# Optimization experiments

Hardware: AMD Instinct MI355X
Metric: run time of the kernel (lower is better)

## Reference

```python
import jax, jax.numpy as jnp
import numpy as np

NUM_CLASSES = 1000
FEAT_DIM = 512
BATCH = 16384


def setup_inputs() -> dict:
    key = jax.random.key(0)
    k1, k2, k3 = jax.random.split(key, 3)
    x = jax.random.normal(k1, (BATCH, FEAT_DIM), dtype=jnp.float32)
    labels = jax.random.randint(k2, (BATCH,), 0, NUM_CLASSES, dtype=jnp.int64)
    centers = jax.random.normal(k3, (NUM_CLASSES, FEAT_DIM), dtype=jnp.float32)
    margin = jnp.ones((1,), dtype=jnp.float32)
    return {"x": x, "labels": labels, "centers": centers, "margin": margin}


def reference(x, labels, centers, margin):
    # squared euclidean distances: [B, C]
    distmat = (
        jnp.sum(x * x, axis=1, keepdims=True)
        + jnp.sum(centers * centers, axis=1)[None, :]
        - 2.0 * (x @ centers.T)
    )
    B, C = distmat.shape
    onehot = labels[:, None] == jnp.arange(C, dtype=labels.dtype)[None, :]  # [B, C]
    # distance to the true-class center
    dist = jnp.sum(jnp.where(onehot, distmat, 0.0), axis=1)  # [B]
    # min distance over all other classes (mask true class with +inf)
    dist_min = jnp.min(jnp.where(onehot, jnp.inf, distmat), axis=1)  # [B]
    m = margin[0]
    loss = jnp.sum(jnp.maximum(m + dist - dist_min, 0.0)) / B
    return loss
```

## Files before the change

kernel.cpp:

```cpp
#include <hip/hip_runtime.h>
#include <hip/hip_bf16.h>

#define BATCH 16384
#define NCLS  1000
#define NPAD  1024
#define FDIM  512

#define CBLK_STRIDE 266240
#define TAIL_OFF    262144
#define XBLK_STRIDE 262144

typedef __bf16 bf16x8 __attribute__((ext_vector_type(8)));
typedef float  f32x16 __attribute__((ext_vector_type(16)));

#define GLOBAL_AS __attribute__((address_space(1)))
#define LDS_AS    __attribute__((address_space(3)))

#define VMCNT(n) asm volatile("s_waitcnt vmcnt(" #n ")" ::: "memory")
#define LGKM0()  asm volatile("s_waitcnt lgkmcnt(0)" ::: "memory")
#define SBAR()   __builtin_amdgcn_s_barrier()
#define SCHED0() __builtin_amdgcn_sched_barrier(0)

__global__ __launch_bounds__(256) void prep(
    const float* __restrict__ centers, const float* __restrict__ x,
    char* __restrict__ cbt, char* __restrict__ xbt, float* __restrict__ out)
{
    const int bid = blockIdx.x, t = threadIdx.x;
    if (bid == 0 && t == 0) out[0] = 0.f;

    if (bid < 256) {
        const int lane = t & 63;
        const int c = bid * 4 + (t >> 6);
        const int cblk = c >> 8, cl = c & 255;
        char* base = cbt + (size_t)cblk * CBLK_STRIDE;

        float4 f0 = make_float4(0.f, 0.f, 0.f, 0.f);
        float4 f1 = make_float4(0.f, 0.f, 0.f, 0.f);
        if (c < NCLS) {
            f0 = *(const float4*)(centers + (size_t)c * FDIM + lane * 8);
            f1 = *(const float4*)(centers + (size_t)c * FDIM + lane * 8 + 4);
        }
        bf16x8 b;
        b[0] = (__bf16)f0.x; b[1] = (__bf16)f0.y; b[2] = (__bf16)f0.z; b[3] = (__bf16)f0.w;
        b[4] = (__bf16)f1.x; b[5] = (__bf16)f1.y; b[6] = (__bf16)f1.z; b[7] = (__bf16)f1.w;
        *(bf16x8*)(base + (lane >> 3) * 32768 + (lane & 7) * 4096 + cl * 16) = b;

        float ssum = f0.x*f0.x + f0.y*f0.y + f0.z*f0.z + f0.w*f0.w
                   + f1.x*f1.x + f1.y*f1.y + f1.z*f1.z + f1.w*f1.w;
        #pragma unroll
        for (int o = 32; o > 0; o >>= 1) ssum += __shfl_down(ssum, o);
        if (lane == 0) {
            const float hf = (c < NCLS) ? (-0.5f * ssum) : -1e30f;
            const __bf16 h = (__bf16)hf;
            const __bf16 l = (c < NCLS) ? (__bf16)(hf - (float)h) : (__bf16)0.f;
            bf16x8 tl;
            #pragma unroll
            for (int e = 0; e < 8; ++e) tl[e] = (__bf16)0.f;
            tl[0] = h; tl[1] = l;
            *(bf16x8*)(base + TAIL_OFF + cl * 16) = tl;
        }
    } else {
        const int pid  = bid - 256;
        const int bblk = pid >> 3, s = pid & 7;
        const float* src = x + (size_t)(bblk * 256 + t) * FDIM + s * 64;
        float4 f[16];
        #pragma unroll
        for (int j = 0; j < 16; ++j) f[j] = *(const float4*)(src + j * 4);
        char* dst = xbt + (size_t)bblk * XBLK_STRIDE + s * 32768 + t * 16;
        #pragma unroll
        for (int c = 0; c < 8; ++c) {
            bf16x8 b;
            b[0] = (__bf16)f[c*2].x;   b[1] = (__bf16)f[c*2].y;
            b[2] = (__bf16)f[c*2].z;   b[3] = (__bf16)f[c*2].w;
            b[4] = (__bf16)f[c*2+1].x; b[5] = (__bf16)f[c*2+1].y;
            b[6] = (__bf16)f[c*2+1].z; b[7] = (__bf16)f[c*2+1].w;
            *(bf16x8*)(dst + c * 4096) = b;
        }
    }
}

__global__ __launch_bounds__(512, 1) void trip_main(
    const int* __restrict__ labels, const char* __restrict__ cbt,
    const char* __restrict__ xbt, float* __restrict__ mxp,
    float* __restrict__ dap)
{
    extern __shared__ char lds[];
    const int t    = threadIdx.x;
    const int lane = t & 63;
    const int w    = t >> 6;
    const int wN   = w & 3, wM = w >> 2;
    const int l31  = lane & 31, hi = lane >> 5;
    const int bid  = blockIdx.x;
    const int cblk = bid >> 6;
    const int bblk = bid & 63;
    const int class0 = cblk * 256;
    const int row0   = bblk * 256;
    const char* cbB  = cbt + (size_t)cblk * CBLK_STRIDE;
    const char* xbB  = xbt + (size_t)bblk * XBLK_STRIDE;

    auto stageAu = [&](int T, int u) {
        const int off = u * 8192 + t * 16;
        __builtin_amdgcn_global_load_lds(
            (const GLOBAL_AS void*)(cbB + T * 32768 + off),
            (LDS_AS void*)(lds + (T & 1) * 32768 + off), 16, 0, 0);
    };

    f32x16 acc[4][2];
    #pragma unroll
    for (int mi = 0; mi < 4; ++mi)
        #pragma unroll
        for (int ni = 0; ni < 2; ++ni)
            #pragma unroll
            for (int r = 0; r < 16; ++r) acc[mi][ni][r] = 0.f;

    bf16x8 bE[4][2], bO[4][2];

    const int lab0 = labels[row0 + wN * 64 + l31];
    const int lab1 = labels[row0 + wN * 64 + 32 + l31];
    if (t < 256) {
        const char* src = cbB + TAIL_OFF + t * 16;
        char* dst = lds + 65536 + t * 16;
        __builtin_amdgcn_global_load_lds((const GLOBAL_AS void*)src,
                                         (LDS_AS void*)dst, 16, 0, 0);
    }
    #pragma unroll
    for (int u = 0; u < 4; ++u) stageAu(0, u);
    #pragma unroll
    for (int u = 0; u < 4; ++u) {
        const char* bsrc = xbB + (u * 2 + hi) * 4096 + (wN * 64 + l31) * 16;
        bE[u][0] = *(const bf16x8*)(bsrc);
        bE[u][1] = *(const bf16x8*)(bsrc + 512);
    }
    VMCNT(0);
    SBAR(); SCHED0();

    #pragma unroll
    for (int T = 0; T < 8; ++T) {
        const char* A = lds + (T & 1) * 32768;
        auto& bCur = (T & 1) ? bO : bE;
        auto& bNxt = (T & 1) ? bE : bO;
        #pragma unroll
        for (int u = 0; u < 4; ++u) {
            if (T < 7)       { VMCNT(6); }
            else if (u == 0) { VMCNT(6); }
            else if (u == 1) { VMCNT(3); }
            else if (u == 2) { VMCNT(0); }
            const int chunk = u * 2 + hi;
            bf16x8 a0 = *(const bf16x8*)(A + chunk * 4096 + (wM * 128 +  0 + l31) * 16);
            bf16x8 a1 = *(const bf16x8*)(A + chunk * 4096 + (wM * 128 + 32 + l31) * 16);
            bf16x8 a2 = *(const bf16x8*)(A + chunk * 4096 + (wM * 128 + 64 + l31) * 16);
            bf16x8 a3 = *(const bf16x8*)(A + chunk * 4096 + (wM * 128 + 96 + l31) * 16);
            if (T < 7) {
                stageAu(T + 1, u);
                const char* bsrc = xbB + (T + 1) * 32768 + chunk * 4096
                                 + (wN * 64 + l31) * 16;
                bNxt[u][0] = *(const bf16x8*)(bsrc);
                bNxt[u][1] = *(const bf16x8*)(bsrc + 512);
            }
            SBAR();
            LGKM0();
            SCHED0();
            __builtin_amdgcn_s_setprio(1);
            acc[0][0] = __builtin_amdgcn_mfma_f32_32x32x16_bf16(a0, bCur[u][0], acc[0][0], 0, 0, 0);
            acc[0][1] = __builtin_amdgcn_mfma_f32_32x32x16_bf16(a0, bCur[u][1], acc[0][1], 0, 0, 0);
            acc[1][0] = __builtin_amdgcn_mfma_f32_32x32x16_bf16(a1, bCur[u][0], acc[1][0], 0, 0, 0);
            acc[1][1] = __builtin_amdgcn_mfma_f32_32x32x16_bf16(a1, bCur[u][1], acc[1][1], 0, 0, 0);
            acc[2][0] = __builtin_amdgcn_mfma_f32_32x32x16_bf16(a2, bCur[u][0], acc[2][0], 0, 0, 0);
            acc[2][1] = __builtin_amdgcn_mfma_f32_32x32x16_bf16(a2, bCur[u][1], acc[2][1], 0, 0, 0);
            acc[3][0] = __builtin_amdgcn_mfma_f32_32x32x16_bf16(a3, bCur[u][0], acc[3][0], 0, 0, 0);
            acc[3][1] = __builtin_amdgcn_mfma_f32_32x32x16_bf16(a3, bCur[u][1], acc[3][1], 0, 0, 0);
            __builtin_amdgcn_s_setprio(0);
            SBAR();
            SCHED0();
        }
    }

    {
        const char* T = lds + 65536;
        bf16x8 bt;
        #pragma unroll
        for (int e = 0; e < 8; ++e) bt[e] = (__bf16)0.f;
        if (hi == 0) { bt[0] = (__bf16)1.0f; bt[1] = (__bf16)1.0f; }
        #pragma unroll
        for (int mi = 0; mi < 4; ++mi) {
            bf16x8 a = *(const bf16x8*)(T + (wM * 128 + mi * 32 + l31) * 16);
            #pragma unroll
            for (int ni = 0; ni < 2; ++ni)
                acc[mi][ni] = __builtin_amdgcn_mfma_f32_32x32x16_bf16(
                    a, bt, acc[mi][ni], 0, 0, 0);
        }
    }

    const int labBase = class0 + wM * 128 + hi * 4;
    const int labA0 = lab0 - labBase;
    const int labA1 = lab1 - labBase;
    float MX0 = -3e38f, MX1 = -3e38f, DA0 = -3e38f, DA1 = -3e38f;
    #pragma unroll
    for (int mi = 0; mi < 4; ++mi) {
        #pragma unroll
        for (int r = 0; r < 16; ++r) {
            const int pat = mi * 32 + (r & 3) + 8 * (r >> 2);
            {
                const float a = acc[mi][0][r];
                const bool is = (labA0 == pat);
                MX0 = fmaxf(MX0, is ? -3e38f : a);
                DA0 = is ? a : DA0;
            }
            {
                const float a = acc[mi][1][r];
                const bool is = (labA1 == pat);
                MX1 = fmaxf(MX1, is ? -3e38f : a);
                DA1 = is ? a : DA1;
            }
        }
    }
    MX0 = fmaxf(MX0, __shfl_xor(MX0, 32));
    DA0 = fmaxf(DA0, __shfl_xor(DA0, 32));
    MX1 = fmaxf(MX1, __shfl_xor(MX1, 32));
    DA1 = fmaxf(DA1, __shfl_xor(DA1, 32));

    float* sc = (float*)lds;
    const int i0 = (wN * 2 + 0) * 32 + l31;
    const int i1 = (wN * 2 + 1) * 32 + l31;
    __syncthreads();
    if (wM == 1 && hi == 0) {
        sc[i0] = MX0; sc[256 + i0] = DA0;
        sc[i1] = MX1; sc[256 + i1] = DA1;
    }
    __syncthreads();
    if (wM == 0 && hi == 0) {
        const float M0 = fmaxf(MX0, sc[i0]),  D0 = fmaxf(DA0, sc[256 + i0]);
        const float M1 = fmaxf(MX1, sc[i1]),  D1 = fmaxf(DA1, sc[256 + i1]);
        const int rg = row0 + wN * 64 + l31;
        mxp[cblk * BATCH + rg]      = M0;
        dap[cblk * BATCH + rg]      = D0;
        mxp[cblk * BATCH + rg + 32] = M1;
        dap[cblk * BATCH + rg + 32] = D1;
    }
}

__global__ __launch_bounds__(256) void combine(
    const float* __restrict__ mxp, const float* __restrict__ dap,
    const float* __restrict__ margin, float* __restrict__ out)
{
    const int t = threadIdx.x;
    const int row = blockIdx.x * 256 + t;
    float mx = fmaxf(fmaxf(mxp[row], mxp[BATCH + row]),
                     fmaxf(mxp[2 * BATCH + row], mxp[3 * BATCH + row]));
    float da = fmaxf(fmaxf(dap[row], dap[BATCH + row]),
                     fmaxf(dap[2 * BATCH + row], dap[3 * BATCH + row]));
    float loss = fmaxf(margin[0] - 2.f * da + 2.f * mx, 0.f);
    __shared__ float red[4];
    #pragma unroll
    for (int o = 32; o > 0; o >>= 1) loss += __shfl_down(loss, o);
    if ((t & 63) == 0) red[t >> 6] = loss;
    __syncthreads();
    if (t == 0)
        atomicAdd(out, (red[0] + red[1] + red[2] + red[3]) * (1.0f / BATCH));
}

extern "C" void kernel_launch(void* const* d_in, const int* in_sizes, int n_in,
                              void* d_out, int out_size, void* d_ws, size_t ws_size,
                              hipStream_t stream)
{
    const float* x       = (const float*)d_in[0];
    const int*   labels  = (const int*)d_in[1];
    const float* centers = (const float*)d_in[2];
    const float* margin  = (const float*)d_in[3];
    float* out = (float*)d_out;

    char* ws = (char*)d_ws;
    char*  cbt  = ws;
    char*  xbt  = ws + 1064960;
    float* mxp  = (float*)(ws + 17842176);
    float* dap  = (float*)(ws + 18104320);

    (void)hipFuncSetAttribute((const void*)trip_main,
                              hipFuncAttributeMaxDynamicSharedMemorySize, 69632);

    prep<<<768, 256, 0, stream>>>(centers, x, cbt, xbt, out);
    trip_main<<<256, 512, 69632, stream>>>(labels, cbt, xbt, mxp, dap);
    combine<<<64, 256, 0, stream>>>(mxp, dap, margin, out);
}
```

Measured before the change: 34.86 us.

## Fuse prep, main and combine kernels into one cooperative launch with grid syncs

Merges the bf16 conversion prep kernel, the main MFMA distance/min kernel and the combine reduction into a single cooperative kernel of 256 blocks separated by grid-wide syncs. This removes two kernel launches and the gaps between them. Prep work is redistributed so each 512-thread block converts two x slices and four center rows. The cost is two grid barriers, plus the prep phase now running on only 256 blocks, and more per-block atomics in the final reduction.

```diff
diff --git a/kernel.cpp b/kernel.cpp
--- a/kernel.cpp
+++ b/kernel.cpp
@@ -1,5 +1,8 @@
 #include <hip/hip_runtime.h>
+#include <hip/hip_cooperative_groups.h>
 #include <hip/hip_bf16.h>
+
+namespace cg = cooperative_groups;
 
 #define BATCH 16384
 #define NCLS  1000
@@ -21,18 +24,41 @@
 #define SBAR()   __builtin_amdgcn_s_barrier()
 #define SCHED0() __builtin_amdgcn_sched_barrier(0)
 
-__global__ __launch_bounds__(256) void prep(
-    const float* __restrict__ centers, const float* __restrict__ x,
-    char* __restrict__ cbt, char* __restrict__ xbt, float* __restrict__ out)
+__global__ __launch_bounds__(512, 1) void trip_fused(
+    const float* __restrict__ x, const int* __restrict__ labels,
+    const float* __restrict__ centers, const float* __restrict__ margin,
+    float* __restrict__ out, char* __restrict__ cbt, char* __restrict__ xbt,
+    float* __restrict__ mxp, float* __restrict__ dap)
 {
-    const int bid = blockIdx.x, t = threadIdx.x;
+    extern __shared__ char lds[];
+    const int t    = threadIdx.x;
+    const int bid  = blockIdx.x;
+
     if (bid == 0 && t == 0) out[0] = 0.f;
-
-    if (bid < 256) {
+    {
+        const int unit = bid * 2 + (t >> 8);
+        const int ubblk = unit >> 3, s = unit & 7;
+        const int tt = t & 255;
+        const float* src = x + (size_t)(ubblk * 256 + tt) * FDIM + s * 64;
+        float4 f[16];
+        #pragma unroll
+        for (int j = 0; j < 16; ++j) f[j] = *(const float4*)(src + j * 4);
+        char* dst = xbt + (size_t)ubblk * XBLK_STRIDE + s * 32768 + tt * 16;
+        #pragma unroll
+        for (int c = 0; c < 8; ++c) {
+            bf16x8 b;
+            b[0] = (__bf16)f[c*2].x;   b[1] = (__bf16)f[c*2].y;
+            b[2] = (__bf16)f[c*2].z;   b[3] = (__bf16)f[c*2].w;
+            b[4] = (__bf16)f[c*2+1].x; b[5] = (__bf16)f[c*2+1].y;
+            b[6] = (__bf16)f[c*2+1].z; b[7] = (__bf16)f[c*2+1].w;
+            *(bf16x8*)(dst + c * 4096) = b;
+        }
+    }
+    if (t < 256) {
         const int lane = t & 63;
         const int c = bid * 4 + (t >> 6);
-        const int cblk = c >> 8, cl = c & 255;
-        char* base = cbt + (size_t)cblk * CBLK_STRIDE;
+        const int ccblk = c >> 8, cl = c & 255;
+        char* base = cbt + (size_t)ccblk * CBLK_STRIDE;
 
         float4 f0 = make_float4(0.f, 0.f, 0.f, 0.f);
         float4 f1 = make_float4(0.f, 0.f, 0.f, 0.f);
@@ -59,38 +85,14 @@
             tl[0] = h; tl[1] = l;
             *(bf16x8*)(base + TAIL_OFF + cl * 16) = tl;
         }
-    } else {
-        const int pid  = bid - 256;
-        const int bblk = pid >> 3, s = pid & 7;
-        const float* src = x + (size_t)(bblk * 256 + t) * FDIM + s * 64;
-        float4 f[16];
-        #pragma unroll
-        for (int j = 0; j < 16; ++j) f[j] = *(const float4*)(src + j * 4);
-        char* dst = xbt + (size_t)bblk * XBLK_STRIDE + s * 32768 + t * 16;
-        #pragma unroll
-        for (int c = 0; c < 8; ++c) {
-            bf16x8 b;
-            b[0] = (__bf16)f[c*2].x;   b[1] = (__bf16)f[c*2].y;
-            b[2] = (__bf16)f[c*2].z;   b[3] = (__bf16)f[c*2].w;
-            b[4] = (__bf16)f[c*2+1].x; b[5] = (__bf16)f[c*2+1].y;
-            b[6] = (__bf16)f[c*2+1].z; b[7] = (__bf16)f[c*2+1].w;
-            *(bf16x8*)(dst + c * 4096) = b;
-        }
-    }
-}
-
-__global__ __launch_bounds__(512, 1) void trip_main(
-    const int* __restrict__ labels, const char* __restrict__ cbt,
-    const char* __restrict__ xbt, float* __restrict__ mxp,
-    float* __restrict__ dap)
-{
-    extern __shared__ char lds[];
-    const int t    = threadIdx.x;
+    }
+
+    cg::this_grid().sync();
+
     const int lane = t & 63;
     const int w    = t >> 6;
     const int wN   = w & 3, wM = w >> 2;
     const int l31  = lane & 31, hi = lane >> 5;
-    const int bid  = blockIdx.x;
     const int cblk = bid >> 6;
     const int bblk = bid & 63;
     const int class0 = cblk * 256;
@@ -237,26 +239,20 @@
         mxp[cblk * BATCH + rg + 32] = M1;
         dap[cblk * BATCH + rg + 32] = D1;
     }
-}
-
-__global__ __launch_bounds__(256) void combine(
-    const float* __restrict__ mxp, const float* __restrict__ dap,
-    const float* __restrict__ margin, float* __restrict__ out)
-{
-    const int t = threadIdx.x;
-    const int row = blockIdx.x * 256 + t;
-    float mx = fmaxf(fmaxf(mxp[row], mxp[BATCH + row]),
-                     fmaxf(mxp[2 * BATCH + row], mxp[3 * BATCH + row]));
-    float da = fmaxf(fmaxf(dap[row], dap[BATCH + row]),
-                     fmaxf(dap[2 * BATCH + row], dap[3 * BATCH + row]));
-    float loss = fmaxf(margin[0] - 2.f * da + 2.f * mx, 0.f);
-    __shared__ float red[4];
-    #pragma unroll
-    for (int o = 32; o > 0; o >>= 1) loss += __shfl_down(loss, o);
-    if ((t & 63) == 0) red[t >> 6] = loss;
-    __syncthreads();
-    if (t == 0)
-        atomicAdd(out, (red[0] + red[1] + red[2] + red[3]) * (1.0f / BATCH));
+
+    cg::this_grid().sync();
+
+    if (bid < 64 && t < 256) {
+        const int row = bid * 256 + t;
+        float mx = fmaxf(fmaxf(mxp[row], mxp[BATCH + row]),
+                         fmaxf(mxp[2 * BATCH + row], mxp[3 * BATCH + row]));
+        float da = fmaxf(fmaxf(dap[row], dap[BATCH + row]),
+                         fmaxf(dap[2 * BATCH + row], dap[3 * BATCH + row]));
+        float loss = fmaxf(margin[0] - 2.f * da + 2.f * mx, 0.f);
+        #pragma unroll
+        for (int o = 32; o > 0; o >>= 1) loss += __shfl_down(loss, o);
+        if ((t & 63) == 0) atomicAdd(out, loss * (1.0f / BATCH));
+    }
 }
 
 extern "C" void kernel_launch(void* const* d_in, const int* in_sizes, int n_in,
@@ -275,10 +271,12 @@
     float* mxp  = (float*)(ws + 17842176);
     float* dap  = (float*)(ws + 18104320);
 
-    (void)hipFuncSetAttribute((const void*)trip_main,
+    (void)hipFuncSetAttribute((const void*)trip_fused,
                               hipFuncAttributeMaxDynamicSharedMemorySize, 69632);
 
-    prep<<<768, 256, 0, stream>>>(centers, x, cbt, xbt, out);
-    trip_main<<<256, 512, 69632, stream>>>(labels, cbt, xbt, mxp, dap);
-    combine<<<64, 256, 0, stream>>>(mxp, dap, margin, out);
+    void* args[] = { (void*)&x, (void*)&labels, (void*)&centers, (void*)&margin,
+                     (void*)&out, (void*)&cbt, (void*)&xbt,
+                     (void*)&mxp, (void*)&dap };
+    (void)hipLaunchCooperativeKernel((const void*)trip_fused,
+                                     dim3(256), dim3(512), args, 69632, stream);
 }
```

After: 117.2 us. +236.1%, slower.
